# Kernel tuning notes

Hardware: AMD Instinct MI355X
Metric: run time of the kernel (lower is better)

The kernel has to match this reference:

```python
import jax, jax.numpy as jnp
import numpy as np
from jax import lax

EPS = 1e-5
B, C, H, W = 16, 256, 56, 56
HEADS, DIM_K, DIM_U, DIM_OUT = 4, 16, 4, 256
DIM_V = DIM_OUT // HEADS  # 64
R = 15


def setup_inputs() -> dict:
    key = jax.random.key(0)
    ks = jax.random.split(key, 16)
    s = 0.05
    return {
        "x": jax.random.normal(ks[0], (B, C, H, W), jnp.float32),
        "Wq": jax.random.normal(ks[1], (C, HEADS * DIM_K), jnp.float32) * s,
        "Wk": jax.random.normal(ks[2], (C, DIM_U * DIM_K), jnp.float32) * s,
        "Wv": jax.random.normal(ks[3], (C, DIM_U * DIM_V), jnp.float32) * s,
        "pos_w": jax.random.normal(ks[4], (DIM_K, DIM_U, 1, R, R), jnp.float32) * s,
        "pos_b": jax.random.normal(ks[5], (DIM_K,), jnp.float32) * s,
        "gq": jax.random.uniform(ks[6], (HEADS * DIM_K,), jnp.float32),
        "bq": jax.random.normal(ks[7], (HEADS * DIM_K,), jnp.float32) * s,
        "mq": jax.random.normal(ks[8], (HEADS * DIM_K,), jnp.float32) * s,
        "vq": jax.random.uniform(ks[9], (HEADS * DIM_K,), jnp.float32) + 0.5,
        "gv": jax.random.uniform(ks[10], (DIM_U * DIM_V,), jnp.float32),
        "bv": jax.random.normal(ks[11], (DIM_U * DIM_V,), jnp.float32) * s,
        "mv": jax.random.normal(ks[12], (DIM_U * DIM_V,), jnp.float32) * s,
        "vv": jax.random.uniform(ks[13], (DIM_U * DIM_V,), jnp.float32) + 0.5,
    }


def _bn(x, gamma, beta, mean, var):
    # inference-mode BatchNorm over channel dim (axis=1), x: [b,c,h,w]
    inv = gamma / jnp.sqrt(var + EPS)
    return x * inv[None, :, None, None] + (beta - mean * inv)[None, :, None, None]


def reference(x, Wq, Wk, Wv, pos_w, pos_b, gq, bq, mq, vq, gv, bv, mv, vv):
    b, c, hh, ww = x.shape
    n = hh * ww
    h, dk, u, dv = HEADS, DIM_K, DIM_U, DIM_V
    # 1x1 convs (channels_first) == channel matmuls
    q = jnp.einsum('bchw,cd->bdhw', x, Wq)
    k = jnp.einsum('bchw,cd->bdhw', x, Wk)
    v = jnp.einsum('bchw,cd->bdhw', x, Wv)
    q = _bn(q, gq, bq, mq, vq)
    v = _bn(v, gv, bv, mv, vv)
    # rearranges: 'b (h k) hh ww -> b h k (hh ww)', 'b (u k) hh ww -> b u k n', 'b (u v) hh ww -> b u v n'
    q = q.reshape(b, h, dk, n)
    k = k.reshape(b, u, dk, n)
    v = v.reshape(b, u, dv, n)
    k = jax.nn.softmax(k, axis=-1)  # keras Softmax default axis=-1 (positions)
    # content lambda
    Lc = jnp.einsum('bukm,buvm->bkv', k, v)
    Yc = jnp.einsum('bhkn,bkv->bnhv', q, Lc)
    # position lambda: conv3d over (v,hh,ww) with kernel (1,r,r), pad spatial only
    v5 = v.reshape(b, u, dv, hh, ww)  # [N, C=u, D=v, H, W]
    p = R // 2
    Lp = lax.conv_general_dilated(
        v5, pos_w, window_strides=(1, 1, 1),
        padding=[(0, 0), (p, p), (p, p)],
        dimension_numbers=('NCDHW', 'OIDHW', 'NCDHW'))
    Lp = Lp + pos_b[None, :, None, None, None]  # [b, k, v, hh, ww]
    Lp = Lp.reshape(b, dk, dv, n)
    Yp = jnp.einsum('bhkn,bkvn->bnhv', q, Lp)
    Y = Yc + Yp  # [b, n, h, v]
    # 'b (hh ww) h v -> b (h v) hh ww'
    out = Y.reshape(b, hh, ww, h, dv).transpose(0, 3, 4, 1, 2).reshape(b, h * dv, hh, ww)
    return out
```

## Files before the change

### kernel.cpp

```cpp
#include <hip/hip_runtime.h>
#include <cstdint>
#include <cstddef>

#define NB   16
#define NC   256
#define NPIX 3136
#define NW   56
#define EPSV 1e-5f

#define BSTR     (384 * NPIX)
#define OFF_VP   (128 * NPIX)
#define VROWD    36
#define VPLANE   (56 * VROWD)
#define OFF_PARTB 917504

#define OFF_AB   0u
#define OFF_BNA  49152u
#define OFF_BNB  49536u
#define OFF_WT   49920u
#define OFF_KS   58112u
#define OFF_LC   59136u
#define OFF_Y    75520u

typedef short bf16x8 __attribute__((ext_vector_type(8)));
typedef float f32x4  __attribute__((ext_vector_type(4)));
typedef float f32x16 __attribute__((ext_vector_type(16)));

__device__ __forceinline__ uint32_t f2bf(float f) {
  uint32_t x = __float_as_uint(f);
  uint32_t r = x + 0x7fffu + ((x >> 16) & 1u);
  return r >> 16;
}
__device__ __forceinline__ uint32_t pk_trunc(float a, float b) {
  return (__float_as_uint(a) >> 16) | (__float_as_uint(b) & 0xffff0000u);
}

__device__ __forceinline__ float fetchW(const float* Wq, const float* Wk,
                                        const float* Wv, int m, int c) {
  if (m < 64)  return Wq[c * 64 + m];
  if (m < 128) return Wk[c * 64 + (m - 64)];
  return Wv[c * 256 + (m - 128)];
}

__global__ void prep_kernel(const float* __restrict__ Wq, const float* __restrict__ Wk,
                            const float* __restrict__ Wv, const float* __restrict__ pos_w,
                            const float* __restrict__ gq, const float* __restrict__ bq,
                            const float* __restrict__ mq, const float* __restrict__ vq,
                            const float* __restrict__ gv, const float* __restrict__ bv,
                            const float* __restrict__ mv, const float* __restrict__ vv,
                            float* __restrict__ ws) {
  int d = blockIdx.x;
  int c = threadIdx.x;
  int i = d * 256 + c;
  if (i < 49152) {
    int dgt = i >> 12, rem = i & 4095;
    int kc = rem >> 8, rem2 = rem & 255;
    int lane = rem2 >> 2, dp = rem2 & 3;
    int m = dgt * 32 + (lane & 31);
    int k0 = kc * 16 + (lane >> 5) * 8 + dp * 2;
    float w0 = fetchW(Wq, Wk, Wv, m, k0);
    float w1 = fetchW(Wq, Wk, Wv, m, k0 + 1);
    ((uint32_t*)(ws + OFF_AB))[i] = f2bf(w0) | (f2bf(w1) << 16);
  }
  if (c == 0) {
    float sa, sb;
    if (d < 64)        { float inv = gq[d] / sqrtf(vq[d] + EPSV); sa = inv; sb = bq[d] - mq[d] * inv; }
    else if (d < 128)  { sa = 1.0f; sb = 0.0f; }
    else               { int j = d - 128; float inv = gv[j] / sqrtf(vv[j] + EPSV); sa = inv; sb = bv[j] - mv[j] * inv; }
    ws[OFF_BNA + d] = sa;
    ws[OFF_BNB + d] = sb;
  }
  if (i < 8192) {
    int chunk = i >> 8, rem = i & 255, lane = rem >> 2, dp = rem & 3;
    int quad = lane >> 4, k = lane & 15;
    int u = chunk >> 3, t = chunk & 7;
    int dh = 2 * t + (quad >> 1);
    int dwb = (quad & 1) * 8 + dp * 2;
    float w0 = (dh < 15 && dwb     < 15) ? pos_w[k * 900 + u * 225 + dh * 15 + dwb]     : 0.0f;
    float w1 = (dh < 15 && dwb + 1 < 15) ? pos_w[k * 900 + u * 225 + dh * 15 + dwb + 1] : 0.0f;
    ((uint32_t*)(ws + OFF_WT))[i] = f2bf(w0) | (f2bf(w1) << 16);
  }
  if (i < 1024) ws[OFF_KS + i] = 0.0f;
  for (int g = i; g < 4096 * 56; g += 98304) {
    int plane = g / 56, r = g - plane * 56;
    int bb = plane >> 8, d2 = plane & 255;
    uint32_t* row = (uint32_t*)(ws + OFF_Y) + (size_t)bb * BSTR + OFF_VP
                    + (size_t)d2 * VPLANE + r * VROWD;
    uint4 z; z.x = 0; z.y = 0; z.z = 0; z.w = 0;
    *(uint4*)(row)      = z;
    *(uint4*)(row + 32) = z;
  }
}

__launch_bounds__(256, 2)
__global__ void qkv_mfma(const float* __restrict__ x, const float* __restrict__ wsc,
                         float* __restrict__ Y) {
  __shared__ uint32_t X[64 * 128];
  __shared__ float BNs[768];
  int tid = threadIdx.x;
  int n0 = blockIdx.x * 64, b = blockIdx.y;
  for (int i = tid; i < 768; i += 256) BNs[i] = wsc[OFF_BNA + i];
  const size_t xb = (size_t)b * NC * NPIX;
#pragma unroll
  for (int it = 0; it < 4; ++it) {
    int n2 = tid & 31;
    int cp4 = it * 8 + (tid >> 5);
    const float* xp = x + xb + (size_t)(cp4 * 8) * NPIX + n0 + n2 * 2;
    float2 ld[8];
#pragma unroll
    for (int j = 0; j < 8; ++j) ld[j] = *(const float2*)(xp + (size_t)j * NPIX);
    uint32_t e0, e1, e2, e3, o0, o1, o2, o3;
    e0 = f2bf(ld[0].x) | (f2bf(ld[1].x) << 16);
    e1 = f2bf(ld[2].x) | (f2bf(ld[3].x) << 16);
    e2 = f2bf(ld[4].x) | (f2bf(ld[5].x) << 16);
    e3 = f2bf(ld[6].x) | (f2bf(ld[7].x) << 16);
    o0 = f2bf(ld[0].y) | (f2bf(ld[1].y) << 16);
    o1 = f2bf(ld[2].y) | (f2bf(ld[3].y) << 16);
    o2 = f2bf(ld[4].y) | (f2bf(ld[5].y) << 16);
    o3 = f2bf(ld[6].y) | (f2bf(ld[7].y) << 16);
    int ne = 2 * n2, no = ne + 1;
    uint4 ve; ve.x = e0; ve.y = e1; ve.z = e2; ve.w = e3;
    uint4 vo; vo.x = o0; vo.y = o1; vo.z = o2; vo.w = o3;
    *(uint4*)(X + ne * 128 + ((cp4 ^ (ne & 31)) << 2)) = ve;
    *(uint4*)(X + no * 128 + ((cp4 ^ (no & 31)) << 2)) = vo;
  }
  __syncthreads();
  int lane = tid & 63, w = tid >> 6;
  int n31 = lane & 31, h5 = lane >> 5;
  f32x16 acc[3][2];
#pragma unroll
  for (int dt = 0; dt < 3; ++dt)
#pragma unroll
    for (int nt = 0; nt < 2; ++nt)
#pragma unroll
      for (int e = 0; e < 16; ++e) acc[dt][nt][e] = 0.0f;
  const uint4* AB = (const uint4*)(wsc + OFF_AB);
#pragma unroll 4
  for (int kc = 0; kc < 16; ++kc) {
    bf16x8 af[3];
#pragma unroll
    for (int dt = 0; dt < 3; ++dt) {
      union { uint4 q; bf16x8 v; } tmp;
      tmp.q = AB[(size_t)(((w * 3 + dt) * 16 + kc)) * 64 + lane];
      af[dt] = tmp.v;
    }
#pragma unroll
    for (int nt = 0; nt < 2; ++nt) {
      union { uint4 q; bf16x8 v; } bu;
      bu.q = *(const uint4*)(X + (nt * 32 + n31) * 128 + (((2 * kc + h5) ^ n31) << 2));
#pragma unroll
      for (int dt = 0; dt < 3; ++dt)
        acc[dt][nt] = __builtin_amdgcn_mfma_f32_32x32x16_bf16(af[dt], bu.v, acc[dt][nt], 0, 0, 0);
    }
  }
#pragma unroll
  for (int dt = 0; dt < 3; ++dt) {
    int dgt = w * 3 + dt;
    float sa[16], sb[16];
#pragma unroll
    for (int g = 0; g < 4; ++g) {
      *(float4*)(sa + g * 4) = *(const float4*)(BNs + dgt * 32 + g * 8 + h5 * 4);
      *(float4*)(sb + g * 4) = *(const float4*)(BNs + 384 + dgt * 32 + g * 8 + h5 * 4);
    }
#pragma unroll
    for (int nt = 0; nt < 2; ++nt) {
      int pix = n0 + nt * 32 + n31;
      if (dgt < 2) {
        uint2* qb2 = (uint2*)(Y + (size_t)b * BSTR);
#pragma unroll
        for (int g = 0; g < 4; ++g) {
          float y0 = fmaf(acc[dt][nt][4 * g + 0], sa[4 * g + 0], sb[4 * g + 0]);
          float y1 = fmaf(acc[dt][nt][4 * g + 1], sa[4 * g + 1], sb[4 * g + 1]);
          float y2 = fmaf(acc[dt][nt][4 * g + 2], sa[4 * g + 2], sb[4 * g + 2]);
          float y3 = fmaf(acc[dt][nt][4 * g + 3], sa[4 * g + 3], sb[4 * g + 3]);
          uint2 val;
          val.x = f2bf(y0) | (f2bf(y1) << 16);
          val.y = f2bf(y2) | (f2bf(y3) << 16);
          qb2[(size_t)(dgt * 8 + 2 * g + h5) * NPIX + pix] = val;
        }
      } else if (dgt < 4) {
#pragma unroll
        for (int g = 0; g < 4; ++g)
#pragma unroll
          for (int ki = 0; ki < 4; ++ki) {
            int d = dgt * 32 + 8 * g + 4 * h5 + ki;
            Y[((size_t)b * 384 + d) * NPIX + pix] =
                fmaf(acc[dt][nt][4 * g + ki], sa[4 * g + ki], sb[4 * g + ki]);
          }
      } else {
        int pr = pix / NW, pc = pix - pr * NW;
        int ridx = pr * 72 + 8 + pc;
        unsigned short* vp = (unsigned short*)(Y + (size_t)b * BSTR + OFF_VP);
#pragma unroll
        for (int g = 0; g < 4; ++g)
#pragma unroll
          for (int ki = 0; ki < 4; ++ki) {
            int d2 = dgt * 32 + 8 * g + 4 * h5 + ki - 128;
            float yv = fmaf(acc[dt][nt][4 * g + ki], sa[4 * g + ki], sb[4 * g + ki]);
            vp[(size_t)d2 * 4032 + ridx] = (unsigned short)f2bf(yv);
          }
      }
    }
  }
}

__launch_bounds__(256)
__global__ void lc_mfma(float* __restrict__ Y, float* __restrict__ ws) {
  __shared__ float R[4096];
  __shared__ float Rs[64];
  int bx = blockIdx.x, u = blockIdx.y, b = blockIdx.z;
  int tid = threadIdx.x;
  int lane = tid & 63, w = tid >> 6;
  int col = lane & 15, quad = lane >> 4;
  int slot = bx * 4 + w;
  const float* krow = Y + ((size_t)(b * 384 + 64 + u * 16 + col)) * NPIX;
  const uint32_t* vpb = (const uint32_t*)(Y + (size_t)b * BSTR + OFF_VP)
                        + (size_t)(u * 64 + col) * VPLANE;
  f32x4 acc[4];
#pragma unroll
  for (int vt = 0; vt < 4; ++vt) acc[vt] = (f32x4){0.f, 0.f, 0.f, 0.f};
  float ssum = 0.0f;
  for (int c = slot; c < 126; c += 64) {
    int p0 = c * 32 + quad * 8;
    int row = p0 / 72;
    int pc = p0 - row * 72;
    bool valid = (unsigned)(pc - 8) < 56u;
    float4 k0, k1;
    if (valid) {
      const float* kp = krow + row * NW + pc - 8;
      k0 = *(const float4*)(kp);
      k1 = *(const float4*)(kp + 4);
    } else {
      k0.x = k0.y = k0.z = k0.w = -1e30f;
      k1 = k0;
    }
    float e0 = __expf(k0.x), e1 = __expf(k0.y), e2 = __expf(k0.z), e3 = __expf(k0.w);
    float e4 = __expf(k1.x), e5 = __expf(k1.y), e6 = __expf(k1.z), e7 = __expf(k1.w);
    ssum += (e0 + e1 + e2 + e3) + (e4 + e5 + e6 + e7);
    union { uint32_t d[4]; bf16x8 v; } kb;
    kb.d[0] = pk_trunc(e0, e1);
    kb.d[1] = pk_trunc(e2, e3);
    kb.d[2] = pk_trunc(e4, e5);
    kb.d[3] = pk_trunc(e6, e7);
    int vdw = c * 16 + quad * 4;
#pragma unroll
    for (int vt = 0; vt < 4; ++vt) {
      union { uint4 q; bf16x8 v; } vb;
      vb.q = *(const uint4*)(vpb + (size_t)(vt * 16) * VPLANE + vdw);
      acc[vt] = __builtin_amdgcn_mfma_f32_16x16x32_bf16(vb.v, kb.v, acc[vt], 0, 0, 0);
    }
  }
  ssum += __shfl_xor(ssum, 16);
  ssum += __shfl_xor(ssum, 32);
#pragma unroll
  for (int vt = 0; vt < 4; ++vt)
#pragma unroll
    for (int r = 0; r < 4; ++r)
      R[w * 1024 + vt * 256 + quad * 64 + r * 16 + col] = acc[vt][r];
  if (lane < 16) Rs[w * 16 + col] = ssum;
  __syncthreads();
  float* P = Y + (size_t)b * BSTR + OFF_PARTB + (size_t)(u * 16 + bx) * 1024;
  float4 s0 = *(const float4*)(R + tid * 4);
  float4 s1 = *(const float4*)(R + 1024 + tid * 4);
  float4 s2 = *(const float4*)(R + 2048 + tid * 4);
  float4 s3 = *(const float4*)(R + 3072 + tid * 4);
  float4 tot;
  tot.x = (s0.x + s1.x) + (s2.x + s3.x);
  tot.y = (s0.y + s1.y) + (s2.y + s3.y);
  tot.z = (s0.z + s1.z) + (s2.z + s3.z);
  tot.w = (s0.w + s1.w) + (s2.w + s3.w);
  *(float4*)(P + tid * 4) = tot;
  if (tid < 16)
    atomicAdd(&ws[OFF_KS + b * 64 + u * 16 + tid],
              (Rs[tid] + Rs[16 + tid]) + (Rs[32 + tid] + Rs[48 + tid]));
}

__global__ void lc_reduce(const float* __restrict__ Y, float* __restrict__ ws) {
  int i = blockIdx.x, b = blockIdx.y;
  int t = threadIdx.x;
  __shared__ float invS[64];
  if (t < 64) invS[t] = 1.0f / ws[OFF_KS + b * 64 + t];
  __syncthreads();
  int idx = i * 256 + t;
  int k = idx & 15;
  const float* P = Y + (size_t)b * BSTR + OFF_PARTB;
  float tot = 0.0f;
#pragma unroll
  for (int u = 0; u < 4; ++u) {
    float su = 0.0f;
#pragma unroll
    for (int s = 0; s < 16; ++s) su += P[(size_t)(u * 16 + s) * 1024 + idx];
    tot += su * invS[u * 16 + k];
  }
  ws[OFF_LC + (b * 16 + k) * 64 + (idx >> 4)] = tot;
}

#define ROWS    29
#define RSTR2   72
#define UPITCH2 2088
#define LDSW2   8352

template<int PPLO, int PPHI>
__device__ __forceinline__ void conv_accum(const uint32_t* __restrict__ S,
                                           const uint4* __restrict__ wt,
                                           int abase, int lane, f32x4* acc) {
#pragma unroll 1
  for (int u = 0; u < 4; ++u) {
    bf16x8 wf[8];
#pragma unroll
    for (int t = 0; t < 8; ++t) {
      union { uint4 q; bf16x8 v; } tmp;
      tmp.q = wt[(u * 8 + t) * 64 + lane];
      wf[t] = tmp.v;
    }
    int au = u * UPITCH2 + abase;
#pragma unroll
    for (int PP = PPLO; PP < PPHI; ++PP) {
      int a = au + PP * (2 * RSTR2);
      union { uint32_t u4[4]; bf16x8 v8; } bu;
      bu.u4[0] = S[a];     bu.u4[1] = S[a + 2];
      bu.u4[2] = S[a + 4]; bu.u4[3] = S[a + 6];
#pragma unroll
      for (int t = 0; t < 8; ++t) {
        int q = PP - t;
        if (q >= 0 && q < 7)
          acc[q] = __builtin_amdgcn_mfma_f32_16x16x32_bf16(wf[t], bu.v8, acc[q], 0, 0, 0);
      }
    }
  }
}

__launch_bounds__(512, 4)
__global__ void pos_lambda_mfma(const float* __restrict__ Y, const float* __restrict__ wsc,
                                const float* __restrict__ pos_b, float* __restrict__ out) {
  __shared__ __attribute__((aligned(16))) uint32_t S[LDSW2];
  int v = blockIdx.x, b = blockIdx.y, band = blockIdx.z;
  int rb = band * 14;
  int tid = threadIdx.x;
  const uint32_t* vpad = (const uint32_t*)(Y + (size_t)b * BSTR + OFF_VP);
  for (int ii = tid; ii < 1044; ii += 512) {
    int u = ii / 261;
    int rem = ii - u * 261;
    int row = rem / 9;
    int j3 = rem - row * 9;
    int gr = rb + row - 7;
    uint32_t d0 = 0, d1 = 0, d2 = 0, d3 = 0, d4 = 0;
    if ((unsigned)gr < (unsigned)NW) {
      const uint32_t* pr32 = vpad + (size_t)(u * 64 + v) * VPLANE + gr * VROWD + 4 * j3;
      d0 = pr32[0]; d1 = pr32[1]; d2 = pr32[2]; d3 = pr32[3]; d4 = pr32[4];
    }
    uint32_t* dst = S + u * UPITCH2 + row * RSTR2 + 8 * j3;
    uint4 w0, w1;
    w0.x = __builtin_amdgcn_alignbit(d1, d0, 16);  w0.y = d1;
    w0.z = __builtin_amdgcn_alignbit(d2, d1, 16);  w0.w = d2;
    w1.x = __builtin_amdgcn_alignbit(d3, d2, 16);  w1.y = d3;
    w1.z = __builtin_amdgcn_alignbit(d4, d3, 16);  w1.w = d4;
    *(uint4*)(dst)     = w0;
    *(uint4*)(dst + 4) = w1;
  }
  __syncthreads();
  int lane = tid & 63, wid = tid >> 6;
  int quad = lane >> 4, n = lane & 15;
  int dhp = quad >> 1;
  int ct = wid & 3, p = wid >> 2;
  int cb = (ct == 3) ? 40 : ct * 16;
  int sb = cb + n + (quad & 1) * 8;
  int abase = (p + dhp) * RSTR2 + sb;
  const uint4* wt = (const uint4*)(wsc + OFF_WT);
  float lcq[4];
#pragma unroll
  for (int r = 0; r < 4; ++r) {
    int k = quad * 4 + r;
    lcq[r] = wsc[OFF_LC + (b * 16 + k) * 64 + v] + pos_b[k];
  }
  f32x4 acc[7];
#pragma unroll
  for (int q = 0; q < 7; ++q) {
    acc[q][0] = lcq[0]; acc[q][1] = lcq[1]; acc[q][2] = lcq[2]; acc[q][3] = lcq[3];
  }
  if (band == 0)      conv_accum<3, 14>(S, wt, abase, lane, acc);
  else if (band == 3) conv_accum<0, 11>(S, wt, abase, lane, acc);
  else                conv_accum<0, 14>(S, wt, abase, lane, acc);

  const uint2* qb2 = (const uint2*)(Y + (size_t)b * BSTR);
#pragma unroll
  for (int q = 0; q < 7; ++q) {
    int rr = rb + p + 2 * q;
    int pix = rr * NW + cb + n;
    float m0 = acc[q][0], m1 = acc[q][1];
    float m2 = acc[q][2], m3 = acc[q][3];
    float pp[4];
#pragma unroll
    for (int j = 0; j < 4; ++j) {
      int h = quad ^ j;
      uint2 qd = qb2[(h * 4 + quad) * NPIX + pix];
      float q0 = __uint_as_float(qd.x << 16);
      float q1 = __uint_as_float(qd.x & 0xffff0000u);
      float q2 = __uint_as_float(qd.y << 16);
      float q3 = __uint_as_float(qd.y & 0xffff0000u);
      pp[j] = fmaf(q0, m0, fmaf(q1, m1, fmaf(q2, m2, q3 * m3)));
    }
    float t0 = pp[0] + __shfl_xor(pp[1], 16);
    float t2 = pp[2] + __shfl_xor(pp[3], 16);
    float y  = t0 + __shfl_xor(t2, 32);
    out[((size_t)(b * 256 + quad * 64 + v)) * NPIX + pix] = y;
  }
}

extern "C" void kernel_launch(void* const* d_in, const int* in_sizes, int n_in,
                              void* d_out, int out_size, void* d_ws, size_t ws_size,
                              hipStream_t stream) {
  const float* x     = (const float*)d_in[0];
  const float* Wq    = (const float*)d_in[1];
  const float* Wk    = (const float*)d_in[2];
  const float* Wv    = (const float*)d_in[3];
  const float* pos_w = (const float*)d_in[4];
  const float* pos_b = (const float*)d_in[5];
  const float* gq    = (const float*)d_in[6];
  const float* bq    = (const float*)d_in[7];
  const float* mq    = (const float*)d_in[8];
  const float* vq    = (const float*)d_in[9];
  const float* gv    = (const float*)d_in[10];
  const float* bv    = (const float*)d_in[11];
  const float* mv    = (const float*)d_in[12];
  const float* vv    = (const float*)d_in[13];
  float* ws  = (float*)d_ws;
  float* out = (float*)d_out;
  float* Y   = ws + OFF_Y;

  prep_kernel<<<dim3(384), 256, 0, stream>>>(Wq, Wk, Wv, pos_w, gq, bq, mq, vq,
                                             gv, bv, mv, vv, ws);
  qkv_mfma<<<dim3(49, 16), 256, 0, stream>>>(x, ws, Y);
  lc_mfma<<<dim3(16, 4, 16), 256, 0, stream>>>(Y, ws);
  lc_reduce<<<dim3(4, 16), 256, 0, stream>>>(Y, ws);
  pos_lambda_mfma<<<dim3(64, 16, 4), 512, 0, stream>>>(Y, ws, pos_b, out);
}
```

Baseline: 257.3 us.

## Transpose MFMA operands for K/V epilogue and split LDS conv tile by parity

After: 260.7 us. About the same (+1.3%).

```diff
diff --git a/kernel.cpp b/kernel.cpp
--- a/kernel.cpp
+++ b/kernel.cpp
@@ -135,69 +135,126 @@
 #pragma unroll
       for (int e = 0; e < 16; ++e) acc[dt][nt][e] = 0.0f;
   const uint4* AB = (const uint4*)(wsc + OFF_AB);
+  if (w == 0) {
 #pragma unroll 4
-  for (int kc = 0; kc < 16; ++kc) {
-    bf16x8 af[3];
+    for (int kc = 0; kc < 16; ++kc) {
+      bf16x8 af[3];
+#pragma unroll
+      for (int dt = 0; dt < 3; ++dt) {
+        union { uint4 q; bf16x8 v; } tmp;
+        tmp.q = AB[(size_t)((dt * 16 + kc)) * 64 + lane];
+        af[dt] = tmp.v;
+      }
+#pragma unroll
+      for (int nt = 0; nt < 2; ++nt) {
+        union { uint4 q; bf16x8 v; } bu;
+        bu.q = *(const uint4*)(X + (nt * 32 + n31) * 128 + (((2 * kc + h5) ^ n31) << 2));
+#pragma unroll
+        for (int dt = 0; dt < 3; ++dt)
+          acc[dt][nt] = __builtin_amdgcn_mfma_f32_32x32x16_bf16(af[dt], bu.v, acc[dt][nt], 0, 0, 0);
+      }
+    }
+  } else {
+#pragma unroll 4
+    for (int kc = 0; kc < 16; ++kc) {
+      bf16x8 af[3];
+#pragma unroll
+      for (int dt = 0; dt < 3; ++dt) {
+        union { uint4 q; bf16x8 v; } tmp;
+        tmp.q = AB[(size_t)(((w * 3 + dt) * 16 + kc)) * 64 + lane];
+        af[dt] = tmp.v;
+      }
+#pragma unroll
+      for (int nt = 0; nt < 2; ++nt) {
+        union { uint4 q; bf16x8 v; } bu;
+        bu.q = *(const uint4*)(X + (nt * 32 + n31) * 128 + (((2 * kc + h5) ^ n31) << 2));
+#pragma unroll
+        for (int dt = 0; dt < 3; ++dt)
+          acc[dt][nt] = __builtin_amdgcn_mfma_f32_32x32x16_bf16(bu.v, af[dt], acc[dt][nt], 0, 0, 0);
+      }
+    }
+  }
+  if (w == 0) {
 #pragma unroll
     for (int dt = 0; dt < 3; ++dt) {
-      union { uint4 q; bf16x8 v; } tmp;
-      tmp.q = AB[(size_t)(((w * 3 + dt) * 16 + kc)) * 64 + lane];
-      af[dt] = tmp.v;
-    }
-#pragma unroll
-    for (int nt = 0; nt < 2; ++nt) {
-      union { uint4 q; bf16x8 v; } bu;
-      bu.q = *(const uint4*)(X + (nt * 32 + n31) * 128 + (((2 * kc + h5) ^ n31) << 2));
-#pragma unroll
-      for (int dt = 0; dt < 3; ++dt)
-        acc[dt][nt] = __builtin_amdgcn_mfma_f32_32x32x16_bf16(af[dt], bu.v, acc[dt][nt], 0, 0, 0);
-    }
-  }
-#pragma unroll
-  for (int dt = 0; dt < 3; ++dt) {
-    int dgt = w * 3 + dt;
-    float sa[16], sb[16];
-#pragma unroll
-    for (int g = 0; g < 4; ++g) {
-      *(float4*)(sa + g * 4) = *(const float4*)(BNs + dgt * 32 + g * 8 + h5 * 4);
-      *(float4*)(sb + g * 4) = *(const float4*)(BNs + 384 + dgt * 32 + g * 8 + h5 * 4);
-    }
-#pragma unroll
-    for (int nt = 0; nt < 2; ++nt) {
-      int pix = n0 + nt * 32 + n31;
-      if (dgt < 2) {
-        uint2* qb2 = (uint2*)(Y + (size_t)b * BSTR);
-#pragma unroll
-        for (int g = 0; g < 4; ++g) {
-          float y0 = fmaf(acc[dt][nt][4 * g + 0], sa[4 * g + 0], sb[4 * g + 0]);
-          float y1 = fmaf(acc[dt][nt][4 * g + 1], sa[4 * g + 1], sb[4 * g + 1]);
-          float y2 = fmaf(acc[dt][nt][4 * g + 2], sa[4 * g + 2], sb[4 * g + 2]);
-          float y3 = fmaf(acc[dt][nt][4 * g + 3], sa[4 * g + 3], sb[4 * g + 3]);
-          uint2 val;
-          val.x = f2bf(y0) | (f2bf(y1) << 16);
-          val.y = f2bf(y2) | (f2bf(y3) << 16);
-          qb2[(size_t)(dgt * 8 + 2 * g + h5) * NPIX + pix] = val;
+      int dgt = dt;
+      float sa[16], sb[16];
+#pragma unroll
+      for (int g = 0; g < 4; ++g) {
+        *(float4*)(sa + g * 4) = *(const float4*)(BNs + dgt * 32 + g * 8 + h5 * 4);
+        *(float4*)(sb + g * 4) = *(const float4*)(BNs + 384 + dgt * 32 + g * 8 + h5 * 4);
+      }
+#pragma unroll
+      for (int nt = 0; nt < 2; ++nt) {
+        int pix = n0 + nt * 32 + n31;
+        if (dgt < 2) {
+          uint2* qb2 = (uint2*)(Y + (size_t)b * BSTR);
+#pragma unroll
+          for (int g = 0; g < 4; ++g) {
+            float y0 = fmaf(acc[dt][nt][4 * g + 0], sa[4 * g + 0], sb[4 * g + 0]);
+            float y1 = fmaf(acc[dt][nt][4 * g + 1], sa[4 * g + 1], sb[4 * g + 1]);
+            float y2 = fmaf(acc[dt][nt][4 * g + 2], sa[4 * g + 2], sb[4 * g + 2]);
+            float y3 = fmaf(acc[dt][nt][4 * g + 3], sa[4 * g + 3], sb[4 * g + 3]);
+            uint2 val;
+            val.x = f2bf(y0) | (f2bf(y1) << 16);
+            val.y = f2bf(y2) | (f2bf(y3) << 16);
+            qb2[(size_t)(dgt * 8 + 2 * g + h5) * NPIX + pix] = val;
+          }
+        } else {
+#pragma unroll
+          for (int g = 0; g < 4; ++g)
+#pragma unroll
+            for (int ki = 0; ki < 4; ++ki) {
+              int d = dgt * 32 + 8 * g + 4 * h5 + ki;
+              Y[((size_t)b * 384 + d) * NPIX + pix] = acc[dt][nt][4 * g + ki];
+            }
         }
-      } else if (dgt < 4) {
-#pragma unroll
-        for (int g = 0; g < 4; ++g)
-#pragma unroll
-          for (int ki = 0; ki < 4; ++ki) {
-            int d = dgt * 32 + 8 * g + 4 * h5 + ki;
-            Y[((size_t)b * 384 + d) * NPIX + pix] =
-                fmaf(acc[dt][nt][4 * g + ki], sa[4 * g + ki], sb[4 * g + ki]);
+      }
+    }
+  } else {
+    int prr[2][4], pcc[2][4];
+#pragma unroll
+    for (int nt = 0; nt < 2; ++nt)
+#pragma unroll
+      for (int j = 0; j < 4; ++j) {
+        int pb = n0 + nt * 32 + 8 * j + 4 * h5;
+        prr[nt][j] = pb / NW;
+        pcc[nt][j] = pb - prr[nt][j] * NW;
+      }
+    unsigned short* vp = (unsigned short*)(Y + (size_t)b * BSTR + OFF_VP);
+#pragma unroll
+    for (int dt = 0; dt < 3; ++dt) {
+      int dgt = w * 3 + dt;
+      if (dgt == 3) {
+        float* kp = Y + ((size_t)(b * 384) + 96 + n31) * NPIX;
+#pragma unroll
+        for (int nt = 0; nt < 2; ++nt)
+#pragma unroll
+          for (int j = 0; j < 4; ++j) {
+            float4 st;
+            st.x = acc[dt][nt][4 * j + 0];
+            st.y = acc[dt][nt][4 * j + 1];
+            st.z = acc[dt][nt][4 * j + 2];
+            st.w = acc[dt][nt][4 * j + 3];
+            *(float4*)(kp + prr[nt][j] * NW + pcc[nt][j]) = st;
           }
       } else {
-        int pr = pix / NW, pc = pix - pr * NW;
-        int ridx = pr * 72 + 8 + pc;
-        unsigned short* vp = (unsigned short*)(Y + (size_t)b * BSTR + OFF_VP);
-#pragma unroll
-        for (int g = 0; g < 4; ++g)
-#pragma unroll
-          for (int ki = 0; ki < 4; ++ki) {
-            int d2 = dgt * 32 + 8 * g + 4 * h5 + ki - 128;
-            float yv = fmaf(acc[dt][nt][4 * g + ki], sa[4 * g + ki], sb[4 * g + ki]);
-            vp[(size_t)d2 * 4032 + ridx] = (unsigned short)f2bf(yv);
+        int d2 = dgt * 32 + n31 - 128;
+        float sa = BNs[dgt * 32 + n31];
+        float sb2 = BNs[384 + dgt * 32 + n31];
+        unsigned short* vpd = vp + (size_t)d2 * 4032;
+#pragma unroll
+        for (int nt = 0; nt < 2; ++nt)
+#pragma unroll
+          for (int j = 0; j < 4; ++j) {
+            float y0 = fmaf(acc[dt][nt][4 * j + 0], sa, sb2);
+            float y1 = fmaf(acc[dt][nt][4 * j + 1], sa, sb2);
+            float y2 = fmaf(acc[dt][nt][4 * j + 2], sa, sb2);
+            float y3 = fmaf(acc[dt][nt][4 * j + 3], sa, sb2);
+            uint2 val;
+            val.x = f2bf(y0) | (f2bf(y1) << 16);
+            val.y = f2bf(y2) | (f2bf(y3) << 16);
+            *(uint2*)(vpd + prr[nt][j] * 72 + 8 + pcc[nt][j]) = val;
           }
       }
     }
@@ -296,14 +353,15 @@
 }
 
 #define ROWS    29
-#define RSTR2   72
-#define UPITCH2 2088
-#define LDSW2   8352
+#define ERSTR   40
+#define EOOFF   1168
+#define UPITCH4 2328
+#define LDSW4   9312
 
 template<int PPLO, int PPHI>
-__device__ __forceinline__ void conv_accum(const uint32_t* __restrict__ S,
+__device__ __forceinline__ void conv_accum(const uint32_t* __restrict__ Sp,
                                            const uint4* __restrict__ wt,
-                                           int abase, int lane, f32x4* acc) {
+                                           int lane, f32x4* acc) {
 #pragma unroll 1
   for (int u = 0; u < 4; ++u) {
     bf16x8 wf[8];
@@ -313,13 +371,14 @@
       tmp.q = wt[(u * 8 + t) * 64 + lane];
       wf[t] = tmp.v;
     }
-    int au = u * UPITCH2 + abase;
+    const uint32_t* Su = Sp + u * UPITCH4;
 #pragma unroll
     for (int PP = PPLO; PP < PPHI; ++PP) {
-      int a = au + PP * (2 * RSTR2);
       union { uint32_t u4[4]; bf16x8 v8; } bu;
-      bu.u4[0] = S[a];     bu.u4[1] = S[a + 2];
-      bu.u4[2] = S[a + 4]; bu.u4[3] = S[a + 6];
+      bu.u4[0] = Su[PP * 80];
+      bu.u4[1] = Su[PP * 80 + 1];
+      bu.u4[2] = Su[PP * 80 + 2];
+      bu.u4[3] = Su[PP * 80 + 3];
 #pragma unroll
       for (int t = 0; t < 8; ++t) {
         int q = PP - t;
@@ -333,7 +392,7 @@
 __launch_bounds__(512, 4)
 __global__ void pos_lambda_mfma(const float* __restrict__ Y, const float* __restrict__ wsc,
                                 const float* __restrict__ pos_b, float* __restrict__ out) {
-  __shared__ __attribute__((aligned(16))) uint32_t S[LDSW2];
+  __shared__ __attribute__((aligned(16))) uint32_t S[LDSW4];
   int v = blockIdx.x, b = blockIdx.y, band = blockIdx.z;
   int rb = band * 14;
   int tid = threadIdx.x;
@@ -347,16 +406,19 @@
     uint32_t d0 = 0, d1 = 0, d2 = 0, d3 = 0, d4 = 0;
     if ((unsigned)gr < (unsigned)NW) {
       const uint32_t* pr32 = vpad + (size_t)(u * 64 + v) * VPLANE + gr * VROWD + 4 * j3;
-      d0 = pr32[0]; d1 = pr32[1]; d2 = pr32[2]; d3 = pr32[3]; d4 = pr32[4];
-    }
-    uint32_t* dst = S + u * UPITCH2 + row * RSTR2 + 8 * j3;
-    uint4 w0, w1;
-    w0.x = __builtin_amdgcn_alignbit(d1, d0, 16);  w0.y = d1;
-    w0.z = __builtin_amdgcn_alignbit(d2, d1, 16);  w0.w = d2;
-    w1.x = __builtin_amdgcn_alignbit(d3, d2, 16);  w1.y = d3;
-    w1.z = __builtin_amdgcn_alignbit(d4, d3, 16);  w1.w = d4;
-    *(uint4*)(dst)     = w0;
-    *(uint4*)(dst + 4) = w1;
+      uint4 q4 = *(const uint4*)pr32;
+      d0 = q4.x; d1 = q4.y; d2 = q4.z; d3 = q4.w;
+      d4 = pr32[4];
+    }
+    uint32_t* dstE = S + u * UPITCH4 + row * ERSTR + 4 * j3;
+    uint4 eo;
+    eo.x = __builtin_amdgcn_alignbit(d1, d0, 16);
+    eo.y = __builtin_amdgcn_alignbit(d2, d1, 16);
+    eo.z = __builtin_amdgcn_alignbit(d3, d2, 16);
+    eo.w = __builtin_amdgcn_alignbit(d4, d3, 16);
+    *(uint4*)(dstE) = eo;
+    uint4 oo; oo.x = d1; oo.y = d2; oo.z = d3; oo.w = d4;
+    *(uint4*)(dstE + EOOFF) = oo;
   }
   __syncthreads();
   int lane = tid & 63, wid = tid >> 6;
@@ -364,8 +426,9 @@
   int dhp = quad >> 1;
   int ct = wid & 3, p = wid >> 2;
   int cb = (ct == 3) ? 40 : ct * 16;
-  int sb = cb + n + (quad & 1) * 8;
-  int abase = (p + dhp) * RSTR2 + sb;
+  int sbb = cb + n + ((quad & 1) << 3);
+  int par = sbb & 1, sidx = sbb >> 1;
+  const uint32_t* Sp = S + (p + dhp) * ERSTR + (par ? EOOFF : 0) + sidx;
   const uint4* wt = (const uint4*)(wsc + OFF_WT);
   float lcq[4];
 #pragma unroll
@@ -378,9 +441,9 @@
   for (int q = 0; q < 7; ++q) {
     acc[q][0] = lcq[0]; acc[q][1] = lcq[1]; acc[q][2] = lcq[2]; acc[q][3] = lcq[3];
   }
-  if (band == 0)      conv_accum<3, 14>(S, wt, abase, lane, acc);
-  else if (band == 3) conv_accum<0, 11>(S, wt, abase, lane, acc);
-  else                conv_accum<0, 14>(S, wt, abase, lane, acc);
+  if (band == 0)      conv_accum<3, 14>(Sp, wt, lane, acc);
+  else if (band == 3) conv_accum<0, 11>(Sp, wt, lane, acc);
+  else                conv_accum<0, 14>(Sp, wt, lane, acc);
 
   const uint2* qb2 = (const uint2*)(Y + (size_t)b * BSTR);
 #pragma unroll
```
